# Kernel tuning notes

Measured on AMD Instinct MI355X. Metric: run time of the kernel, lower is better.

Reference implementation:

```python
import jax, jax.numpy as jnp
import numpy as np

N = 100000
E = 500000
D_IN = 128
D_H = 128
MAX_ITERS = 3  # min(int(T=2.0)+1, 3); step weights all >= 0.5 so no early break


def setup_inputs() -> dict:
    key = jax.random.key(0)
    ks = jax.random.split(key, 7)
    node_feats = jax.random.normal(ks[0], (N, D_IN), dtype=jnp.float32)
    edge_index = jax.random.randint(ks[1], (2, E), 0, N, dtype=jnp.int64)
    init = lambda k, shp, fan: jax.random.normal(k, shp, dtype=jnp.float32) / np.float32(np.sqrt(fan))
    W_s = init(ks[2], (D_H, D_IN), D_IN)        # Linear(d_in, d_h, bias=False)
    W_pc = init(ks[3], (D_H, D_H), D_H)         # Linear(d_h, d_h, bias=False)
    W_edge = init(ks[4], (D_H, 2 * D_H), 2 * D_H)  # Linear(2*d_h, d_h, bias=False)
    W_gate_w = init(ks[5], (1, 2 * D_H), 2 * D_H)  # Linear(2*d_h, 1)
    W_gate_b = jnp.zeros((1,), jnp.float32)
    T = jnp.float32(2.0)  # learnable iteration-count parameter, init tree_iterations
    return dict(node_feats=node_feats, edge_index=edge_index, W_s=W_s, W_pc=W_pc,
                W_edge=W_edge, W_gate_w=W_gate_w, W_gate_b=W_gate_b, T=T)


def _step(h, p_idx, c_idx, W_pc, W_edge, W_gate_w, W_gate_b):
    h_p = h[p_idx]                                   # [E, d_h] gather
    h_c = h[c_idx]                                   # [E, d_h] gather
    ec = jnp.concatenate([h_p, h_c], axis=1)         # [E, 2*d_h]
    msg = ec @ W_edge.T                              # edge projection
    alpha = jax.nn.sigmoid(ec @ W_gate_w.T + W_gate_b)  # [E, 1] gate
    msg = msg * alpha
    # scatter_add into both endpoints (symmetric aggregation)
    agg = jnp.zeros_like(h).at[p_idx].add(msg).at[c_idx].add(msg)
    new_h = jax.nn.relu(agg @ W_pc.T + h)
    return new_h + h  # residual=True


def reference(node_feats, edge_index, W_s, W_pc, W_edge, W_gate_w, W_gate_b, T):
    p_idx, c_idx = edge_index[0], edge_index[1]
    h = node_feats @ W_s.T                           # [N, d_h]
    for step in range(MAX_ITERS):
        w = jax.nn.sigmoid(T - step)                 # learned step weight
        step_h = _step(h, p_idx, c_idx, W_pc, W_edge, W_gate_w, W_gate_b)
        h = h + w * (step_h - h)
    return h  # outputs['hidden'] (dropout is identity in eval)
```

## Files before the change

kernel.cpp:

```cpp
#include <hip/hip_runtime.h>
#include <cstdio>
#include <cstddef>

#define DH 128

typedef _Float16 f16;
typedef __attribute__((ext_vector_type(8))) _Float16 f16x8;
typedef __attribute__((ext_vector_type(4))) _Float16 f16x4;
typedef __attribute__((ext_vector_type(2))) _Float16 f16x2;
typedef __attribute__((ext_vector_type(4))) float    f32x4;
typedef unsigned int u32;

__global__ __launch_bounds__(128) void wc_kernel(const float* __restrict__ Wpc,
                                                 const float* __restrict__ Wedge,
                                                 const float* __restrict__ Ws,
                                                 f16* __restrict__ Bg16,
                                                 f16* __restrict__ Ws16)
{
    int o = blockIdx.x;
    int k = threadIdx.x;
    if (o < 256) {
        int orow = o & 127;
        int col  = (o < 128) ? k : (128 + k);
        float acc = 0.f;
        for (int m = 0; m < 128; ++m)
            acc += Wpc[orow * 128 + m] * Wedge[m * 256 + col];
        Bg16[o * 128 + k] = (f16)acc;
    } else {
        int row = o - 256;
        Ws16[row * 128 + k] = (f16)Ws[row * 128 + k];
    }
}

__global__ __launch_bounds__(256) void prep_k(const int* __restrict__ idx,
                                              int* __restrict__ cnt, int twoE,
                                              const float* __restrict__ x,
                                              f16* __restrict__ x16, int n4)
{
    const int stride = gridDim.x * blockDim.x;
    const int mx = (twoE > n4) ? twoE : n4;
    for (int i = blockIdx.x * blockDim.x + threadIdx.x; i < mx; i += stride) {
        if (i < twoE) atomicAdd(cnt + idx[i], 1);
        if (i < n4) {
            float4 v = ((const float4*)x)[i];
            f16x2 a = {(f16)v.x, (f16)v.y};
            f16x2 b = {(f16)v.z, (f16)v.w};
            ((f16x2*)x16)[2 * i]     = a;
            ((f16x2*)x16)[2 * i + 1] = b;
        }
    }
}

template<int OUT, int NT, bool WF32, bool WF16, bool FUSES>
__global__ __launch_bounds__(256) void mfma_gemm_t(const f16* __restrict__ A16,
                                                   const f16* __restrict__ B16,
                                                   float* __restrict__ Cf,
                                                   f16* __restrict__ Ch,
                                                   const float* __restrict__ wg,
                                                   float* __restrict__ s,
                                                   int M)
{
    const int lane = threadIdx.x & 63;
    const int row0 = blockIdx.x * (NT * 64) + (threadIdx.x >> 6) * (NT * 16);
    const int r = lane & 15, kg = lane >> 4;

    int  mrow[NT];
    bool ok[NT];
    f16x8 a[NT][4];
#pragma unroll
    for (int t = 0; t < NT; ++t) {
        mrow[t] = row0 + t * 16 + r;
        ok[t]   = (mrow[t] < M);
        int ar  = ok[t] ? mrow[t] : M - 1;
        const f16x8* Ap = (const f16x8*)(A16 + (size_t)ar * 128 + kg * 8);
        a[t][0] = Ap[0]; a[t][1] = Ap[4]; a[t][2] = Ap[8]; a[t][3] = Ap[12];
    }

    float sp0[NT], sp1[NT];
    if constexpr (FUSES) {
#pragma unroll
        for (int t = 0; t < NT; ++t) { sp0[t] = 0.f; sp1[t] = 0.f; }
    }

    for (int ct = 0; ct < OUT / 16; ++ct) {
        const f16x8* Bp = (const f16x8*)(B16 + (size_t)(ct * 16 + r) * 128 + kg * 8);
        f16x8 b0 = Bp[0], b1 = Bp[4], b2 = Bp[8], b3 = Bp[12];
        const int o0 = ct * 16 + kg * 4;
        float w0, w1, w2, w3, u0, u1, u2, u3;
        if constexpr (FUSES) {
            w0 = wg[o0]; w1 = wg[o0+1]; w2 = wg[o0+2]; w3 = wg[o0+3];
            u0 = wg[128+o0]; u1 = wg[128+o0+1]; u2 = wg[128+o0+2]; u3 = wg[128+o0+3];
        }
#pragma unroll
        for (int t = 0; t < NT; ++t) {
            f32x4 acc = {0.f, 0.f, 0.f, 0.f};
            acc = __builtin_amdgcn_mfma_f32_16x16x32_f16(b0, a[t][0], acc, 0, 0, 0);
            acc = __builtin_amdgcn_mfma_f32_16x16x32_f16(b1, a[t][1], acc, 0, 0, 0);
            acc = __builtin_amdgcn_mfma_f32_16x16x32_f16(b2, a[t][2], acc, 0, 0, 0);
            acc = __builtin_amdgcn_mfma_f32_16x16x32_f16(b3, a[t][3], acc, 0, 0, 0);
            if (ok[t]) {
                if constexpr (WF32)
                    *(float4*)(Cf + (size_t)mrow[t] * OUT + o0) =
                        make_float4(acc[0], acc[1], acc[2], acc[3]);
                if constexpr (WF16) {
                    f16x4 hv = {(f16)acc[0], (f16)acc[1], (f16)acc[2], (f16)acc[3]};
                    *(f16x4*)(Ch + (size_t)mrow[t] * OUT + o0) = hv;
                }
            }
            if constexpr (FUSES) {
                sp0[t] += acc[0]*w0 + acc[1]*w1 + acc[2]*w2 + acc[3]*w3;
                sp1[t] += acc[0]*u0 + acc[1]*u1 + acc[2]*u2 + acc[3]*u3;
            }
        }
    }
    if constexpr (FUSES) {
#pragma unroll
        for (int t = 0; t < NT; ++t) {
            float p0 = sp0[t], p1 = sp1[t];
            p0 += __shfl_xor(p0, 16); p0 += __shfl_xor(p0, 32);
            p1 += __shfl_xor(p1, 16); p1 += __shfl_xor(p1, 32);
            if (kg == 0 && ok[t])
                *(float2*)(s + 2 * mrow[t]) = make_float2(p0, p1);
        }
    }
}

#define SCAN_B 256
__global__ __launch_bounds__(SCAN_B) void scan1(const int* __restrict__ cnt,
                                                int* __restrict__ bsum, int Nn)
{
    __shared__ int sm[SCAN_B];
    int i = blockIdx.x * SCAN_B + threadIdx.x;
    sm[threadIdx.x] = (i < Nn) ? cnt[i] : 0;
    __syncthreads();
    for (int off = SCAN_B / 2; off > 0; off >>= 1) {
        if (threadIdx.x < off) sm[threadIdx.x] += sm[threadIdx.x + off];
        __syncthreads();
    }
    if (threadIdx.x == 0) bsum[blockIdx.x] = sm[0];
}

__global__ __launch_bounds__(1024) void scan2(int* __restrict__ bsum, int nb,
                                              int* __restrict__ totalOut)
{
    __shared__ int sm[1024];
    int t = threadIdx.x;
    sm[t] = (t < nb) ? bsum[t] : 0;
    __syncthreads();
    for (int off = 1; off < 1024; off <<= 1) {
        int u = (t >= off) ? sm[t - off] : 0;
        __syncthreads();
        sm[t] += u;
        __syncthreads();
    }
    if (t < nb) bsum[t] = (t == 0) ? 0 : sm[t - 1];
    if (t == nb - 1) *totalOut = sm[t];
}

__global__ __launch_bounds__(SCAN_B) void scan3(const int* __restrict__ cnt,
                                                const int* __restrict__ bsum,
                                                int* __restrict__ base,
                                                int* __restrict__ cursor, int Nn)
{
    __shared__ int sm[SCAN_B];
    int i = blockIdx.x * SCAN_B + threadIdx.x;
    int v = (i < Nn) ? cnt[i] : 0;
    sm[threadIdx.x] = v;
    __syncthreads();
    for (int off = 1; off < SCAN_B; off <<= 1) {
        int u = (threadIdx.x >= off) ? sm[threadIdx.x - off] : 0;
        __syncthreads();
        sm[threadIdx.x] += u;
        __syncthreads();
    }
    if (i < Nn) {
        int b = bsum[blockIdx.x] + sm[threadIdx.x] - v;
        base[i] = b;
        cursor[i] = b;
    }
}

__global__ __launch_bounds__(256) void fill_xcd(const int* __restrict__ idx,
                                                int* __restrict__ cursor,
                                                int* __restrict__ adjp,
                                                int E, int Nn)
{
    const int xcd  = blockIdx.x & 7;
    const int gblk = blockIdx.x >> 3;
    const int ngrp = gridDim.x >> 3;
    const int twoE = 2 * E;
    const int lo = xcd * Nn, hi = lo + Nn;
    for (int i = gblk * blockDim.x + threadIdx.x; i < twoE; i += ngrp * blockDim.x) {
        int node = idx[i];
        int n8 = node << 3;
        if (n8 < lo || n8 >= hi) continue;
        int side  = (i >= E);
        int e     = side ? i - E : i;
        int other = side ? idx[e] : idx[E + e];
        int pos = atomicAdd(cursor + node, 1);
        adjp[pos] = other | (side << 31);
    }
}

template<bool LAST>
__global__ __launch_bounds__(256) void agg7(const f16* __restrict__ g16,
                                            const int* __restrict__ adjp,
                                            const int* __restrict__ base,
                                            const float* __restrict__ sIn,
                                            float* __restrict__ sOut,
                                            float* __restrict__ h,
                                            f16* __restrict__ h16,
                                            const float* __restrict__ wg,
                                            const float* __restrict__ gbp,
                                            const float* __restrict__ Tp,
                                            float stepf, int Nn, int twoE)
{
    const int lane = threadIdx.x & 63;
    const int grp  = lane >> 4;
    const int gl   = lane & 15;
    const int wvid = (blockIdx.x * blockDim.x + threadIdx.x) >> 6;
    int n = wvid * 4 + grp;
    const bool nOK = (n < Nn);
    if (n >= Nn) n = Nn - 1;
    const float gb = gbp[0];
    const float w  = 1.f / (1.f + expf(-(Tp[0] - stepf)));
    const int b0 = base[n], b1 = base[n + 1];
    const int deg = b1 - b0;
    const float s1n = sIn[2 * n], s2n = sIn[2 * n + 1];
    const int d0 = gl << 3;

    f16x8 o1 = *(const f16x8*)(g16 + (size_t)n * 256 + d0);
    f16x8 o2 = *(const f16x8*)(g16 + (size_t)n * 256 + 128 + d0);
    float4 hv0 = *(const float4*)(h + (size_t)n * DH + d0);
    float4 hv1 = *(const float4*)(h + (size_t)n * DH + d0 + 4);

    f16x2 acc0 = {(f16)0.f, (f16)0.f};
    f16x2 acc1 = {(f16)0.f, (f16)0.f};
    f16x2 acc2 = {(f16)0.f, (f16)0.f};
    f16x2 acc3 = {(f16)0.f, (f16)0.f};
    float aPl = 0.f, aCl = 0.f;

    union V8 { f16x8 v; f16x2 h2[4]; };
    union AU { u32 w; f16x2 h; unsigned short us[2]; };

    int t = 0;
    while (__any(t * 16 < deg)) {
        const int done = t * 16;
        int m = deg - done; m = (m < 0) ? 0 : ((m > 16) ? 16 : m);
        int midx = b0 + done + ((gl < m) ? gl : ((m > 0) ? m - 1 : 0));
        midx = (midx < twoE - 1) ? midx : (twoE - 1);
        midx = (midx > 0) ? midx : 0;
        int meta  = adjp[midx];
        int other = meta & 0x7FFFFFFF;
        int side  = ((unsigned)meta) >> 31;
        int eoff  = (other << 8) | ((side ^ 1) << 7);
        float sv  = sIn[2 * other + (side ^ 1)];
        float aE  = 1.f / (1.f + expf(-((side ? s2n : s1n) + sv + gb)));
        if (gl >= m) aE = 0.f;
        aPl += side ? 0.f : aE;
        aCl += side ? aE : 0.f;

        AU apk;
        apk.h[0] = (f16)aE;
        apk.us[1] = apk.us[0];

        const int sb = grp << 4;
        for (int j = 0; j < m; j += 8) {
            V8 gv[8]; u32 ap[8];
#pragma unroll
            for (int u = 0; u < 8; ++u) {
                int es = j + u; es = (es < 15) ? es : 15;
                int eo = __shfl(eoff, sb | es);
                ap[u]  = (u32)__shfl((int)apk.w, sb | es);
                gv[u].v = *(const f16x8*)(g16 + (size_t)(unsigned)eo + d0);
            }
#pragma unroll
            for (int u = 0; u < 8; ++u) {
                AU aa; aa.w = ap[u];
                acc0 += aa.h * gv[u].h2[0];
                acc1 += aa.h * gv[u].h2[1];
                acc2 += aa.h * gv[u].h2[2];
                acc3 += aa.h * gv[u].h2[3];
            }
        }
        ++t;
    }

    float a8[8];
    a8[0] = (float)acc0[0]; a8[1] = (float)acc0[1];
    a8[2] = (float)acc1[0]; a8[3] = (float)acc1[1];
    a8[4] = (float)acc2[0]; a8[5] = (float)acc2[1];
    a8[6] = (float)acc3[0]; a8[7] = (float)acc3[1];

    float aP = aPl, aC = aCl;
#pragma unroll
    for (int off = 8; off > 0; off >>= 1) {
        aP += __shfl_xor(aP, off);
        aC += __shfl_xor(aC, off);
    }
#pragma unroll
    for (int i = 0; i < 8; ++i)
        a8[i] += aP * (float)o1[i] + aC * (float)o2[i];

    hv0.x += w * fmaxf(a8[0] + hv0.x, 0.f);
    hv0.y += w * fmaxf(a8[1] + hv0.y, 0.f);
    hv0.z += w * fmaxf(a8[2] + hv0.z, 0.f);
    hv0.w += w * fmaxf(a8[3] + hv0.w, 0.f);
    hv1.x += w * fmaxf(a8[4] + hv1.x, 0.f);
    hv1.y += w * fmaxf(a8[5] + hv1.y, 0.f);
    hv1.z += w * fmaxf(a8[6] + hv1.z, 0.f);
    hv1.w += w * fmaxf(a8[7] + hv1.w, 0.f);

    float p0 = 0.f, p1 = 0.f;
    if (nOK) {
        *(float4*)(h + (size_t)n * DH + d0)     = hv0;
        *(float4*)(h + (size_t)n * DH + d0 + 4) = hv1;
        if constexpr (!LAST) {
            f16x8 h2 = {(f16)hv0.x, (f16)hv0.y, (f16)hv0.z, (f16)hv0.w,
                        (f16)hv1.x, (f16)hv1.y, (f16)hv1.z, (f16)hv1.w};
            *(f16x8*)(h16 + (size_t)n * DH + d0) = h2;
        }
    }
    if constexpr (!LAST) {
        float4 w0a = *(const float4*)(wg + d0);
        float4 w0b = *(const float4*)(wg + d0 + 4);
        float4 w1a = *(const float4*)(wg + 128 + d0);
        float4 w1b = *(const float4*)(wg + 128 + d0 + 4);
        p0 = hv0.x*w0a.x + hv0.y*w0a.y + hv0.z*w0a.z + hv0.w*w0a.w
           + hv1.x*w0b.x + hv1.y*w0b.y + hv1.z*w0b.z + hv1.w*w0b.w;
        p1 = hv0.x*w1a.x + hv0.y*w1a.y + hv0.z*w1a.z + hv0.w*w1a.w
           + hv1.x*w1b.x + hv1.y*w1b.y + hv1.z*w1b.z + hv1.w*w1b.w;
#pragma unroll
        for (int off = 8; off > 0; off >>= 1) {
            p0 += __shfl_xor(p0, off);
            p1 += __shfl_xor(p1, off);
        }
        if (gl == 0 && nOK) *(float2*)(sOut + 2 * n) = make_float2(p0, p1);
    }
}

static inline size_t alignUp(size_t x) { return (x + 255) & ~(size_t)255; }

extern "C" void kernel_launch(void* const* d_in, const int* in_sizes, int n_in,
                              void* d_out, int out_size, void* d_ws, size_t ws_size,
                              hipStream_t stream)
{
    const float* x     = (const float*)d_in[0];
    const int*   idx   = (const int*)d_in[1];
    const float* Ws    = (const float*)d_in[2];
    const float* Wpc   = (const float*)d_in[3];
    const float* Wedge = (const float*)d_in[4];
    const float* Wg    = (const float*)d_in[5];
    const float* Wgb   = (const float*)d_in[6];
    const float* Tp    = (const float*)d_in[7];
    const int Nn = in_sizes[0] / DH;
    const int E  = in_sizes[1] / 2;
    float* h = (float*)d_out;

    const int nb = (Nn + SCAN_B - 1) / SCAN_B;
    if (nb > 1024) { fprintf(stderr, "kernel_launch: Nn too big for scan\n"); return; }

    size_t off = 0;
    char* wsb = (char*)d_ws;
    f16*   g16    = (f16*)  (wsb + off); off = alignUp(off + (size_t)Nn * 256 * 2);
    f16*   h16    = (f16*)  (wsb + off); off = alignUp(off + (size_t)Nn * DH * 2);
    f16*   x16    = (f16*)  (wsb + off); off = alignUp(off + (size_t)Nn * DH * 2);
    f16*   Ws16   = (f16*)  (wsb + off); off = alignUp(off + 128 * 128 * 2);
    f16*   Bg16   = (f16*)  (wsb + off); off = alignUp(off + 256 * 128 * 2);
    float* sA     = (float*)(wsb + off); off = alignUp(off + (size_t)Nn * 2 * 4);
    float* sB     = (float*)(wsb + off); off = alignUp(off + (size_t)Nn * 2 * 4);
    int*   cnt    = (int*)  (wsb + off); off = alignUp(off + (size_t)Nn * 4);
    int*   base   = (int*)  (wsb + off); off = alignUp(off + (size_t)(Nn + 1) * 4);
    int*   cursor = (int*)  (wsb + off); off = alignUp(off + (size_t)Nn * 4);
    int*   bsum   = (int*)  (wsb + off); off = alignUp(off + 1024 * 4);
    int*   adjp   = (int*)  (wsb + off); off = alignUp(off + (size_t)(2 * E + 64) * 4);
    if (off > ws_size) {
        fprintf(stderr, "kernel_launch: ws too small (%zu < %zu)\n", ws_size, off);
        return;
    }

    hipMemsetAsync(cnt, 0, (size_t)Nn * 4, stream);
    prep_k<<<dim3(2048), dim3(256), 0, stream>>>(idx, cnt, 2 * E, x, x16, Nn * DH / 4);
    scan1<<<dim3(nb), dim3(SCAN_B), 0, stream>>>(cnt, bsum, Nn);
    scan2<<<dim3(1), dim3(1024), 0, stream>>>(bsum, nb, base + Nn);
    scan3<<<dim3(nb), dim3(SCAN_B), 0, stream>>>(cnt, bsum, base, cursor, Nn);
    fill_xcd<<<dim3(1280), dim3(256), 0, stream>>>(idx, cursor, adjp, E, Nn);

    wc_kernel<<<dim3(384), dim3(128), 0, stream>>>(Wpc, Wedge, Ws, Bg16, Ws16);
    mfma_gemm_t<128, 2, true, true, true>
        <<<dim3((Nn + 127) / 128), dim3(256), 0, stream>>>(x16, Ws16, h, h16, Wg, sA, Nn);

    const int aggBlocks = (Nn * 16 + 255) / 256;
    float* sCur = sA; float* sNxt = sB;
    for (int step = 0; step < 3; ++step) {
        mfma_gemm_t<256, 4, false, true, false>
            <<<dim3((Nn + 255) / 256), dim3(256), 0, stream>>>(h16, Bg16, nullptr, g16,
                                                               nullptr, nullptr, Nn);
        if (step < 2)
            agg7<false><<<dim3(aggBlocks), dim3(256), 0, stream>>>(g16, adjp, base, sCur,
                                                                   sNxt, h, h16, Wg, Wgb,
                                                                   Tp, (float)step, Nn, 2 * E);
        else
            agg7<true><<<dim3(aggBlocks), dim3(256), 0, stream>>>(g16, adjp, base, sCur,
                                                                  sNxt, h, h16, Wg, Wgb,
                                                                  Tp, (float)step, Nn, 2 * E);
        float* t = sCur; sCur = sNxt; sNxt = t;
    }
}
```

Measured before the change: 417.5 us.

## Drop fp32 hidden state, read x as fp32 in GEMM, merge prep kernels

```diff
diff --git a/kernel.cpp b/kernel.cpp
--- a/kernel.cpp
+++ b/kernel.cpp
@@ -11,11 +11,13 @@
 typedef __attribute__((ext_vector_type(4))) float    f32x4;
 typedef unsigned int u32;
 
-__global__ __launch_bounds__(128) void wc_kernel(const float* __restrict__ Wpc,
-                                                 const float* __restrict__ Wedge,
-                                                 const float* __restrict__ Ws,
-                                                 f16* __restrict__ Bg16,
-                                                 f16* __restrict__ Ws16)
+__global__ __launch_bounds__(128) void prep2(const float* __restrict__ Wpc,
+                                             const float* __restrict__ Wedge,
+                                             const float* __restrict__ Ws,
+                                             f16* __restrict__ Bg16,
+                                             f16* __restrict__ Ws16,
+                                             const int* __restrict__ idx,
+                                             int* __restrict__ cnt, int twoE)
 {
     int o = blockIdx.x;
     int k = threadIdx.x;
@@ -26,33 +28,18 @@
         for (int m = 0; m < 128; ++m)
             acc += Wpc[orow * 128 + m] * Wedge[m * 256 + col];
         Bg16[o * 128 + k] = (f16)acc;
-    } else {
+    } else if (o < 384) {
         int row = o - 256;
         Ws16[row * 128 + k] = (f16)Ws[row * 128 + k];
-    }
-}
-
-__global__ __launch_bounds__(256) void prep_k(const int* __restrict__ idx,
-                                              int* __restrict__ cnt, int twoE,
-                                              const float* __restrict__ x,
-                                              f16* __restrict__ x16, int n4)
-{
-    const int stride = gridDim.x * blockDim.x;
-    const int mx = (twoE > n4) ? twoE : n4;
-    for (int i = blockIdx.x * blockDim.x + threadIdx.x; i < mx; i += stride) {
-        if (i < twoE) atomicAdd(cnt + idx[i], 1);
-        if (i < n4) {
-            float4 v = ((const float4*)x)[i];
-            f16x2 a = {(f16)v.x, (f16)v.y};
-            f16x2 b = {(f16)v.z, (f16)v.w};
-            ((f16x2*)x16)[2 * i]     = a;
-            ((f16x2*)x16)[2 * i + 1] = b;
-        }
-    }
-}
-
-template<int OUT, int NT, bool WF32, bool WF16, bool FUSES>
-__global__ __launch_bounds__(256) void mfma_gemm_t(const f16* __restrict__ A16,
+    } else {
+        const int stride = (gridDim.x - 384) * 128;
+        for (int i = (o - 384) * 128 + k; i < twoE; i += stride)
+            atomicAdd(cnt + idx[i], 1);
+    }
+}
+
+template<int OUT, int NT, bool AF32, bool WF32, bool WF16, bool FUSES>
+__global__ __launch_bounds__(256) void mfma_gemm_t(const void* __restrict__ Avp,
                                                    const f16* __restrict__ B16,
                                                    float* __restrict__ Cf,
                                                    f16* __restrict__ Ch,
@@ -72,8 +59,20 @@
         mrow[t] = row0 + t * 16 + r;
         ok[t]   = (mrow[t] < M);
         int ar  = ok[t] ? mrow[t] : M - 1;
-        const f16x8* Ap = (const f16x8*)(A16 + (size_t)ar * 128 + kg * 8);
-        a[t][0] = Ap[0]; a[t][1] = Ap[4]; a[t][2] = Ap[8]; a[t][3] = Ap[12];
+        if constexpr (AF32) {
+            const float4* Ap = (const float4*)((const float*)Avp + (size_t)ar * 128);
+#pragma unroll
+            for (int q = 0; q < 4; ++q) {
+                float4 f0 = Ap[kg * 2 + q * 8];
+                float4 f1 = Ap[kg * 2 + q * 8 + 1];
+                f16x8 fr = {(f16)f0.x, (f16)f0.y, (f16)f0.z, (f16)f0.w,
+                            (f16)f1.x, (f16)f1.y, (f16)f1.z, (f16)f1.w};
+                a[t][q] = fr;
+            }
+        } else {
+            const f16x8* Ap = (const f16x8*)((const f16*)Avp + (size_t)ar * 128 + kg * 8);
+            a[t][0] = Ap[0]; a[t][1] = Ap[4]; a[t][2] = Ap[8]; a[t][3] = Ap[12];
+        }
     }
 
     float sp0[NT], sp1[NT];
@@ -203,12 +202,12 @@
 }
 
 template<bool LAST>
-__global__ __launch_bounds__(256) void agg7(const f16* __restrict__ g16,
+__global__ __launch_bounds__(256) void agg8(const f16* __restrict__ g16,
                                             const int* __restrict__ adjp,
                                             const int* __restrict__ base,
                                             const float* __restrict__ sIn,
                                             float* __restrict__ sOut,
-                                            float* __restrict__ h,
+                                            float* __restrict__ hOut,
                                             f16* __restrict__ h16,
                                             const float* __restrict__ wg,
                                             const float* __restrict__ gbp,
@@ -231,8 +230,7 @@
 
     f16x8 o1 = *(const f16x8*)(g16 + (size_t)n * 256 + d0);
     f16x8 o2 = *(const f16x8*)(g16 + (size_t)n * 256 + 128 + d0);
-    float4 hv0 = *(const float4*)(h + (size_t)n * DH + d0);
-    float4 hv1 = *(const float4*)(h + (size_t)n * DH + d0 + 4);
+    f16x8 hv16 = *(const f16x8*)(h16 + (size_t)n * DH + d0);
 
     f16x2 acc0 = {(f16)0.f, (f16)0.f};
     f16x2 acc1 = {(f16)0.f, (f16)0.f};
@@ -302,22 +300,23 @@
     for (int i = 0; i < 8; ++i)
         a8[i] += aP * (float)o1[i] + aC * (float)o2[i];
 
-    hv0.x += w * fmaxf(a8[0] + hv0.x, 0.f);
-    hv0.y += w * fmaxf(a8[1] + hv0.y, 0.f);
-    hv0.z += w * fmaxf(a8[2] + hv0.z, 0.f);
-    hv0.w += w * fmaxf(a8[3] + hv0.w, 0.f);
-    hv1.x += w * fmaxf(a8[4] + hv1.x, 0.f);
-    hv1.y += w * fmaxf(a8[5] + hv1.y, 0.f);
-    hv1.z += w * fmaxf(a8[6] + hv1.z, 0.f);
-    hv1.w += w * fmaxf(a8[7] + hv1.w, 0.f);
+    float hf[8];
+#pragma unroll
+    for (int i = 0; i < 8; ++i) {
+        hf[i] = (float)hv16[i];
+        hf[i] += w * fmaxf(a8[i] + hf[i], 0.f);
+    }
 
     float p0 = 0.f, p1 = 0.f;
     if (nOK) {
-        *(float4*)(h + (size_t)n * DH + d0)     = hv0;
-        *(float4*)(h + (size_t)n * DH + d0 + 4) = hv1;
-        if constexpr (!LAST) {
-            f16x8 h2 = {(f16)hv0.x, (f16)hv0.y, (f16)hv0.z, (f16)hv0.w,
-                        (f16)hv1.x, (f16)hv1.y, (f16)hv1.z, (f16)hv1.w};
+        if constexpr (LAST) {
+            *(float4*)(hOut + (size_t)n * DH + d0) =
+                make_float4(hf[0], hf[1], hf[2], hf[3]);
+            *(float4*)(hOut + (size_t)n * DH + d0 + 4) =
+                make_float4(hf[4], hf[5], hf[6], hf[7]);
+        } else {
+            f16x8 h2 = {(f16)hf[0], (f16)hf[1], (f16)hf[2], (f16)hf[3],
+                        (f16)hf[4], (f16)hf[5], (f16)hf[6], (f16)hf[7]};
             *(f16x8*)(h16 + (size_t)n * DH + d0) = h2;
         }
     }
@@ -326,10 +325,10 @@
         float4 w0b = *(const float4*)(wg + d0 + 4);
         float4 w1a = *(const float4*)(wg + 128 + d0);
         float4 w1b = *(const float4*)(wg + 128 + d0 + 4);
-        p0 = hv0.x*w0a.x + hv0.y*w0a.y + hv0.z*w0a.z + hv0.w*w0a.w
-           + hv1.x*w0b.x + hv1.y*w0b.y + hv1.z*w0b.z + hv1.w*w0b.w;
-        p1 = hv0.x*w1a.x + hv0.y*w1a.y + hv0.z*w1a.z + hv0.w*w1a.w
-           + hv1.x*w1b.x + hv1.y*w1b.y + hv1.z*w1b.z + hv1.w*w1b.w;
+        p0 = hf[0]*w0a.x + hf[1]*w0a.y + hf[2]*w0a.z + hf[3]*w0a.w
+           + hf[4]*w0b.x + hf[5]*w0b.y + hf[6]*w0b.z + hf[7]*w0b.w;
+        p1 = hf[0]*w1a.x + hf[1]*w1a.y + hf[2]*w1a.z + hf[3]*w1a.w
+           + hf[4]*w1b.x + hf[5]*w1b.y + hf[6]*w1b.z + hf[7]*w1b.w;
 #pragma unroll
         for (int off = 8; off > 0; off >>= 1) {
             p0 += __shfl_xor(p0, off);
@@ -364,7 +363,6 @@
     char* wsb = (char*)d_ws;
     f16*   g16    = (f16*)  (wsb + off); off = alignUp(off + (size_t)Nn * 256 * 2);
     f16*   h16    = (f16*)  (wsb + off); off = alignUp(off + (size_t)Nn * DH * 2);
-    f16*   x16    = (f16*)  (wsb + off); off = alignUp(off + (size_t)Nn * DH * 2);
     f16*   Ws16   = (f16*)  (wsb + off); off = alignUp(off + 128 * 128 * 2);
     f16*   Bg16   = (f16*)  (wsb + off); off = alignUp(off + 256 * 128 * 2);
     float* sA     = (float*)(wsb + off); off = alignUp(off + (size_t)Nn * 2 * 4);
@@ -380,28 +378,29 @@
     }
 
     hipMemsetAsync(cnt, 0, (size_t)Nn * 4, stream);
-    prep_k<<<dim3(2048), dim3(256), 0, stream>>>(idx, cnt, 2 * E, x, x16, Nn * DH / 4);
+    prep2<<<dim3(2048), dim3(128), 0, stream>>>(Wpc, Wedge, Ws, Bg16, Ws16,
+                                                idx, cnt, 2 * E);
     scan1<<<dim3(nb), dim3(SCAN_B), 0, stream>>>(cnt, bsum, Nn);
     scan2<<<dim3(1), dim3(1024), 0, stream>>>(bsum, nb, base + Nn);
     scan3<<<dim3(nb), dim3(SCAN_B), 0, stream>>>(cnt, bsum, base, cursor, Nn);
     fill_xcd<<<dim3(1280), dim3(256), 0, stream>>>(idx, cursor, adjp, E, Nn);
 
-    wc_kernel<<<dim3(384), dim3(128), 0, stream>>>(Wpc, Wedge, Ws, Bg16, Ws16);
-    mfma_gemm_t<128, 2, true, true, true>
-        <<<dim3((Nn + 127) / 128), dim3(256), 0, stream>>>(x16, Ws16, h, h16, Wg, sA, Nn);
+    mfma_gemm_t<128, 2, true, false, true, true>
+        <<<dim3((Nn + 127) / 128), dim3(256), 0, stream>>>(x, Ws16, nullptr, h16,
+                                                           Wg, sA, Nn);
 
     const int aggBlocks = (Nn * 16 + 255) / 256;
     float* sCur = sA; float* sNxt = sB;
     for (int step = 0; step < 3; ++step) {
-        mfma_gemm_t<256, 4, false, true, false>
+        mfma_gemm_t<256, 4, false, false, true, false>
             <<<dim3((Nn + 255) / 256), dim3(256), 0, stream>>>(h16, Bg16, nullptr, g16,
                                                                nullptr, nullptr, Nn);
         if (step < 2)
-            agg7<false><<<dim3(aggBlocks), dim3(256), 0, stream>>>(g16, adjp, base, sCur,
+            agg8<false><<<dim3(aggBlocks), dim3(256), 0, stream>>>(g16, adjp, base, sCur,
                                                                    sNxt, h, h16, Wg, Wgb,
                                                                    Tp, (float)step, Nn, 2 * E);
         else
-            agg7<true><<<dim3(aggBlocks), dim3(256), 0, stream>>>(g16, adjp, base, sCur,
+            agg8<true><<<dim3(aggBlocks), dim3(256), 0, stream>>>(g16, adjp, base, sCur,
                                                                   sNxt, h, h16, Wg, Wgb,
                                                                   Tp, (float)step, Nn, 2 * E);
         float* t = sCur; sCur = sNxt; sNxt = t;
```

Measured after the change: 385.1 us. 1.08x faster.
